# Kernel optimization log

Hardware: AMD Instinct MI355X
Metric: run time of the kernel (lower is better)

The kernel has to match this reference:

```python
import jax, jax.numpy as jnp
import numpy as np

D = 512        # input_dimension
STEPS = 6      # set2set processing steps
N = 100000     # set size (nodes)


def setup_inputs() -> dict:
    key = jax.random.key(0)
    ks = jax.random.split(key, 7)
    s_in = 1.0 / np.sqrt(2 * D)
    s_h = 1.0 / np.sqrt(D)
    s_p = 1.0 / np.sqrt(D * STEPS)
    return {
        "x": jax.random.normal(ks[0], (N, D), dtype=jnp.float32),
        # PyTorch LSTM params: W_ih [4D, 2D], W_hh [4D, D], gate order i,f,g,o
        "W_ih": jax.random.uniform(ks[1], (4 * D, 2 * D), jnp.float32, -s_in, s_in),
        "W_hh": jax.random.uniform(ks[2], (4 * D, D), jnp.float32, -s_h, s_h),
        "b_ih": jax.random.uniform(ks[3], (4 * D,), jnp.float32, -s_h, s_h),
        "b_hh": jax.random.uniform(ks[4], (4 * D,), jnp.float32, -s_h, s_h),
        # projection Linear(D*STEPS -> D)
        "W_proj": jax.random.uniform(ks[5], (D, D * STEPS), jnp.float32, -s_p, s_p),
        "b_proj": jax.random.uniform(ks[6], (D,), jnp.float32, -s_p, s_p),
    }


def reference(x, W_ih, W_hh, b_ih, b_hh, W_proj, b_proj):
    d = x.shape[1]
    h0 = jnp.zeros((d,), dtype=x.dtype)
    c0 = jnp.zeros((d,), dtype=x.dtype)

    def step(carry, _):
        h, c = carry
        scores = jax.nn.softmax(x @ h)          # [N] attention over the set
        ctx = scores @ x                         # [D] attended context
        inp = jnp.concatenate([ctx, h])          # [2D] lstm input (context, hidden)
        gates = W_ih @ inp + b_ih + W_hh @ h + b_hh  # [4D]
        i, f, g, o = jnp.split(gates, 4)
        i = jax.nn.sigmoid(i)
        f = jax.nn.sigmoid(f)
        g = jnp.tanh(g)
        o = jax.nn.sigmoid(o)
        c_new = f * c + i * g
        h_new = o * jnp.tanh(c_new)
        return (h_new, c_new), ctx

    (_, _), contexts = jax.lax.scan(step, (h0, c0), None, length=STEPS)  # [STEPS, D]
    return jax.nn.softmax(W_proj @ contexts.reshape(-1) + b_proj)  # [D]
```

## Files before the change

### kernel.cpp

```cpp
#include <hip/hip_runtime.h>
#include <math.h>

#define D 512
#define STEPS 6
#define MAXB1 1024

__device__ __forceinline__ float wave_reduce_sum(float v) {
#pragma unroll
    for (int off = 32; off > 0; off >>= 1) v += __shfl_xor(v, off);
    return v;
}

__device__ __forceinline__ float dot8(const float4& a, const float4& b,
                                      const float4& ha, const float4& hb) {
    return a.x*ha.x + a.y*ha.y + a.z*ha.z + a.w*ha.w
         + b.x*hb.x + b.y*hb.y + b.z*hb.z + b.w*hb.w;
}

#define ONLINE(dv, av, bv) do {                                          \
    if ((dv) > m) {                                                      \
        float sc_ = __expf(m - (dv));                                    \
        s *= sc_;                                                        \
        va.x *= sc_; va.y *= sc_; va.z *= sc_; va.w *= sc_;              \
        vb.x *= sc_; vb.y *= sc_; vb.z *= sc_; vb.w *= sc_;              \
        m = (dv);                                                        \
    }                                                                    \
    float w_ = __expf((dv) - m);                                         \
    s += w_;                                                             \
    va.x += w_*(av).x; va.y += w_*(av).y; va.z += w_*(av).z; va.w += w_*(av).w; \
    vb.x += w_*(bv).x; vb.y += w_*(bv).y; vb.z += w_*(bv).z; vb.w += w_*(bv).w; \
} while (0)

__global__ __launch_bounds__(256, 4) void attn_kernel(
    const float* __restrict__ x, const float* __restrict__ h,
    float* __restrict__ pm, float* __restrict__ ps, float* __restrict__ pv, int N)
{
    __shared__ float h_s[D];
    __shared__ float red_v[4][D];
    __shared__ float red_ms[8];
    for (int i = threadIdx.x; i < D; i += 256) h_s[i] = h[i];
    __syncthreads();

    const int wave = threadIdx.x >> 6, lane = threadIdx.x & 63;
    const int nw = gridDim.x << 2;
    const float4 ha = ((const float4*)h_s)[lane];
    const float4 hb = ((const float4*)h_s)[64 + lane];

    float m = -1e30f, s = 0.f;
    float4 va = make_float4(0.f, 0.f, 0.f, 0.f);
    float4 vb = make_float4(0.f, 0.f, 0.f, 0.f);

    int i = (blockIdx.x << 2) + wave;
    const int limit4 = N - 3 * nw;
    for (; i < limit4; i += (nw << 2)) {
        const float4* x0 = (const float4*)(x + (size_t)i * D);
        const float4* x1 = (const float4*)(x + (size_t)(i + nw) * D);
        const float4* x2 = (const float4*)(x + (size_t)(i + 2 * nw) * D);
        const float4* x3 = (const float4*)(x + (size_t)(i + 3 * nw) * D);
        float4 a0 = x0[lane], b0 = x0[64 + lane];
        float4 a1 = x1[lane], b1 = x1[64 + lane];
        float4 a2 = x2[lane], b2 = x2[64 + lane];
        float4 a3 = x3[lane], b3 = x3[64 + lane];
        float d0 = dot8(a0, b0, ha, hb);
        float d1 = dot8(a1, b1, ha, hb);
        float d2 = dot8(a2, b2, ha, hb);
        float d3 = dot8(a3, b3, ha, hb);
#pragma unroll
        for (int off = 32; off > 0; off >>= 1) {
            d0 += __shfl_xor(d0, off);
            d1 += __shfl_xor(d1, off);
            d2 += __shfl_xor(d2, off);
            d3 += __shfl_xor(d3, off);
        }
        ONLINE(d0, a0, b0);
        ONLINE(d1, a1, b1);
        ONLINE(d2, a2, b2);
        ONLINE(d3, a3, b3);
    }
    for (; i < N; i += nw) {
        const float4* x0 = (const float4*)(x + (size_t)i * D);
        float4 a0 = x0[lane], b0 = x0[64 + lane];
        float d0 = dot8(a0, b0, ha, hb);
        d0 = wave_reduce_sum(d0);
        ONLINE(d0, a0, b0);
    }

    ((float4*)red_v[wave])[lane] = va;
    ((float4*)red_v[wave])[64 + lane] = vb;
    if (lane == 0) { red_ms[wave] = m; red_ms[4 + wave] = s; }
    __syncthreads();

    float m0 = red_ms[0], m1 = red_ms[1], m2 = red_ms[2], m3 = red_ms[3];
    float bm = fmaxf(fmaxf(m0, m1), fmaxf(m2, m3));
    float sc0 = __expf(m0 - bm), sc1 = __expf(m1 - bm);
    float sc2 = __expf(m2 - bm), sc3 = __expf(m3 - bm);
    if (threadIdx.x == 0) {
        pm[blockIdx.x] = bm;
        ps[blockIdx.x] = red_ms[4]*sc0 + red_ms[5]*sc1 + red_ms[6]*sc2 + red_ms[7]*sc3;
    }
    const int t = threadIdx.x;
    float v0 = red_v[0][t]*sc0 + red_v[1][t]*sc1 + red_v[2][t]*sc2 + red_v[3][t]*sc3;
    float v1 = red_v[0][t+256]*sc0 + red_v[1][t+256]*sc1
             + red_v[2][t+256]*sc2 + red_v[3][t+256]*sc3;
    pv[(size_t)blockIdx.x * D + t] = v0;
    pv[(size_t)blockIdx.x * D + t + 256] = v1;
}

__global__ __launch_bounds__(256) void combine_kernel(
    const float* __restrict__ pm, const float* __restrict__ ps,
    const float* __restrict__ pv, float* __restrict__ ctx,
    float* __restrict__ ctx_store, int B1)
{
    __shared__ float sm[MAXB1];
    __shared__ float red[8];
    __shared__ float pr[4][64];
    const int tid = threadIdx.x, lane = tid & 63, wave = tid >> 6;

    float lm = -1e30f;
    for (int b = tid; b < B1; b += 256) lm = fmaxf(lm, pm[b]);
#pragma unroll
    for (int off = 32; off > 0; off >>= 1) lm = fmaxf(lm, __shfl_xor(lm, off));
    if (lane == 0) red[wave] = lm;
    __syncthreads();
    float M = fmaxf(fmaxf(red[0], red[1]), fmaxf(red[2], red[3]));

    float lS = 0.f;
    for (int b = tid; b < B1; b += 256) {
        float e = __expf(pm[b] - M);
        sm[b] = e;
        lS += ps[b] * e;
    }
#pragma unroll
    for (int off = 32; off > 0; off >>= 1) lS += __shfl_xor(lS, off);
    if (lane == 0) red[4 + wave] = lS;
    __syncthreads();
    float S = red[4] + red[5] + red[6] + red[7];

    const int d = (blockIdx.x << 6) + lane;
    float acc = 0.f;
    for (int b = wave; b < B1; b += 4)
        acc += pv[(size_t)b * D + d] * sm[b];
    pr[wave][lane] = acc;
    __syncthreads();
    if (tid < 64) {
        float v = (pr[0][lane] + pr[1][lane] + pr[2][lane] + pr[3][lane]) / S;
        int dd = (blockIdx.x << 6) + lane;
        ctx[dd] = v;
        ctx_store[dd] = v;
    }
}

__global__ __launch_bounds__(256) void lstm_kernel(
    const float* __restrict__ W_ih, const float* __restrict__ W_hh,
    const float* __restrict__ b_ih, const float* __restrict__ b_hh,
    const float* __restrict__ ctx, const float* __restrict__ h_in,
    float* __restrict__ h_out, float* __restrict__ c)
{
    __shared__ float inp[2 * D];
    __shared__ float gate[4];
    const int tid = threadIdx.x, lane = tid & 63, g = tid >> 6;
    const int j = blockIdx.x;
    for (int i = tid; i < D; i += 256) { inp[i] = ctx[i]; inp[D + i] = h_in[i]; }
    __syncthreads();

    const int row = (g << 9) + j;
    const float4* wr = (const float4*)(W_ih + (size_t)row * (2 * D));
    float dot = 0.f;
#pragma unroll
    for (int q = 0; q < 4; ++q) {
        float4 w4 = wr[lane + (q << 6)];
        float4 i4 = ((const float4*)inp)[lane + (q << 6)];
        dot += w4.x*i4.x + w4.y*i4.y + w4.z*i4.z + w4.w*i4.w;
    }
    const float4* wr2 = (const float4*)(W_hh + (size_t)row * D);
#pragma unroll
    for (int q = 0; q < 2; ++q) {
        float4 w4 = wr2[lane + (q << 6)];
        float4 i4 = ((const float4*)(inp + D))[lane + (q << 6)];
        dot += w4.x*i4.x + w4.y*i4.y + w4.z*i4.z + w4.w*i4.w;
    }
    dot = wave_reduce_sum(dot);
    if (lane == 0) gate[g] = dot + b_ih[row] + b_hh[row];
    __syncthreads();
    if (tid == 0) {
        float ig = 1.f / (1.f + __expf(-gate[0]));
        float fg = 1.f / (1.f + __expf(-gate[1]));
        float gg = tanhf(gate[2]);
        float og = 1.f / (1.f + __expf(-gate[3]));
        float cn = fg * c[j] + ig * gg;
        c[j] = cn;
        h_out[j] = og * tanhf(cn);
    }
}

__global__ __launch_bounds__(256) void proj_kernel(
    const float* __restrict__ W_proj, const float* __restrict__ b_proj,
    const float* __restrict__ ctxs, float* __restrict__ logits)
{
    __shared__ float cc[STEPS * D];
    const int tid = threadIdx.x, lane = tid & 63, g = tid >> 6;
    for (int i = tid; i < STEPS * D; i += 256) cc[i] = ctxs[i];
    __syncthreads();

    const int row = (blockIdx.x << 2) + g;
    const float4* wr = (const float4*)(W_proj + (size_t)row * (STEPS * D));
    float dot = 0.f;
#pragma unroll
    for (int q = 0; q < 12; ++q) {
        float4 w4 = wr[lane + (q << 6)];
        float4 i4 = ((const float4*)cc)[lane + (q << 6)];
        dot += w4.x*i4.x + w4.y*i4.y + w4.z*i4.z + w4.w*i4.w;
    }
    dot = wave_reduce_sum(dot);
    if (lane == 0) logits[row] = dot + b_proj[row];
}

__global__ void softmax512_kernel(const float* __restrict__ logits, float* __restrict__ out)
{
    __shared__ float red[8];
    const int tid = threadIdx.x, lane = tid & 63, wave = tid >> 6;
    float v = logits[tid];
    float m = v;
#pragma unroll
    for (int off = 32; off > 0; off >>= 1) m = fmaxf(m, __shfl_xor(m, off));
    if (lane == 0) red[wave] = m;
    __syncthreads();
    m = red[0];
#pragma unroll
    for (int k = 1; k < 8; ++k) m = fmaxf(m, red[k]);
    __syncthreads();
    float e = __expf(v - m);
    float s = e;
#pragma unroll
    for (int off = 32; off > 0; off >>= 1) s += __shfl_xor(s, off);
    if (lane == 0) red[wave] = s;
    __syncthreads();
    s = 0.f;
#pragma unroll
    for (int k = 0; k < 8; ++k) s += red[k];
    out[tid] = e / s;
}

extern "C" void kernel_launch(void* const* d_in, const int* in_sizes, int n_in,
                              void* d_out, int out_size, void* d_ws, size_t ws_size,
                              hipStream_t stream)
{
    const float* x      = (const float*)d_in[0];
    const float* W_ih   = (const float*)d_in[1];
    const float* W_hh   = (const float*)d_in[2];
    const float* b_ih   = (const float*)d_in[3];
    const float* b_hh   = (const float*)d_in[4];
    const float* W_proj = (const float*)d_in[5];
    const float* b_proj = (const float*)d_in[6];
    const int N = in_sizes[0] / D;

    float* ws     = (float*)d_ws;
    float* hbuf   = ws;
    float* c      = ws + 1024;
    float* ctx    = ws + 1536;
    float* ctxs   = ws + 2048;
    float* logits = ws + 5120;
    const size_t base = 5632;
    int B1 = MAXB1;
    if ((base + (size_t)B1 * (D + 2)) * sizeof(float) > ws_size) {
        B1 = (int)((ws_size / sizeof(float) - base) / (D + 2));
        if (B1 > MAXB1) B1 = MAXB1;
        if (B1 < 8) B1 = 8;
    }
    float* pm = ws + base;
    float* ps = pm + B1;
    float* pv = ps + B1;

    hipMemsetAsync(d_ws, 0, 1536 * sizeof(float), stream);

    for (int t = 0; t < STEPS; ++t) {
        float* h_in  = hbuf + ((t & 1) << 9);
        float* h_out = hbuf + (((t + 1) & 1) << 9);
        attn_kernel<<<B1, 256, 0, stream>>>(x, h_in, pm, ps, pv, N);
        combine_kernel<<<8, 256, 0, stream>>>(pm, ps, pv, ctx, ctxs + t * D, B1);
        lstm_kernel<<<512, 256, 0, stream>>>(W_ih, W_hh, b_ih, b_hh, ctx, h_in, h_out, c);
    }
    proj_kernel<<<128, 256, 0, stream>>>(W_proj, b_proj, ctxs, logits);
    softmax512_kernel<<<1, 512, 0, stream>>>(logits, (float*)d_out);
}
```

Before: 902.0 us.

## Fuse all set2set stages into one persistent cooperative kernel with grid syncs

Replaces the 20 separate launches (attention, combine and LSTM per step, then projection and softmax) with a single cooperative persistent kernel that uses grid.sync between stages. The goal is to remove per-launch overhead and gaps between launches. In exchange, the attention phase runs with fewer blocks (CUs times occupancy, at most 512), which may reduce memory-level parallelism on the 200MB x stream. The LSTM phase serialises gate rows per block with __syncthreads, and grid barriers cost time. The old multi-kernel path is kept as a fallback if the cooperative launch fails.

```diff
diff --git a/kernel.cpp b/kernel.cpp
--- a/kernel.cpp
+++ b/kernel.cpp
@@ -1,9 +1,21 @@
 #include <hip/hip_runtime.h>
+#include <hip/hip_cooperative_groups.h>
 #include <math.h>
+
+namespace cg = cooperative_groups;
 
 #define D 512
 #define STEPS 6
 #define MAXB1 1024
+
+#define WS_HBUF   0
+#define WS_C      1024
+#define WS_CTX    1536
+#define WS_CTXS   2048
+#define WS_LOGITS 5120
+#define WS_PM     5632
+#define WS_PS     6656
+#define WS_PV     7680
 
 __device__ __forceinline__ float wave_reduce_sum(float v) {
 #pragma unroll
@@ -30,6 +42,7 @@
     va.x += w_*(av).x; va.y += w_*(av).y; va.z += w_*(av).z; va.w += w_*(av).w; \
     vb.x += w_*(bv).x; vb.y += w_*(bv).y; vb.z += w_*(bv).z; vb.w += w_*(bv).w; \
 } while (0)
+
 
 __global__ __launch_bounds__(256, 4) void attn_kernel(
     const float* __restrict__ x, const float* __restrict__ h,
@@ -241,6 +254,238 @@
     out[tid] = e / s;
 }
 
+
+struct SharedU {
+    union {
+        struct { float h_s[D]; float red_v[4][D]; float red_ms[8]; } attn;
+        struct { float sm[512]; float red[8]; float pr[4][64]; } comb;
+        struct { float inp[2 * D]; float gate[4]; } lstm;
+        struct { float cc[STEPS * D]; } proj;
+    };
+};
+
+__global__ __launch_bounds__(256, 2) void s2s_kernel(
+    const float* __restrict__ x,
+    const float* __restrict__ W_ih, const float* __restrict__ W_hh,
+    const float* __restrict__ b_ih, const float* __restrict__ b_hh,
+    const float* __restrict__ W_proj, const float* __restrict__ b_proj,
+    float* __restrict__ out, float* __restrict__ ws, int N)
+{
+    cg::grid_group grid = cg::this_grid();
+    __shared__ SharedU su;
+
+    float* hbuf   = ws + WS_HBUF;
+    float* c      = ws + WS_C;
+    float* ctx    = ws + WS_CTX;
+    float* ctxs   = ws + WS_CTXS;
+    float* logits = ws + WS_LOGITS;
+    float* pm     = ws + WS_PM;
+    float* ps     = ws + WS_PS;
+    float* pv     = ws + WS_PV;
+
+    const int tid = threadIdx.x, lane = tid & 63, wave = tid >> 6;
+    const int bid = blockIdx.x;
+    const int NB = gridDim.x;
+    const int nw = NB << 2;
+
+    if (bid == 0)
+        for (int i = tid; i < 1536; i += 256) ws[i] = 0.f;
+    grid.sync();
+
+    for (int t = 0; t < STEPS; ++t) {
+        float* h_in  = hbuf + ((t & 1) << 9);
+        float* h_out = hbuf + (((t + 1) & 1) << 9);
+
+        {
+            for (int i = tid; i < D; i += 256) su.attn.h_s[i] = h_in[i];
+            __syncthreads();
+            const float4 ha = ((const float4*)su.attn.h_s)[lane];
+            const float4 hb = ((const float4*)su.attn.h_s)[64 + lane];
+
+            float m = -1e30f, s = 0.f;
+            float4 va = make_float4(0.f, 0.f, 0.f, 0.f);
+            float4 vb = make_float4(0.f, 0.f, 0.f, 0.f);
+
+            int i = (bid << 2) + wave;
+            const int limit4 = N - 3 * nw;
+            for (; i < limit4; i += (nw << 2)) {
+                const float4* x0 = (const float4*)(x + (size_t)i * D);
+                const float4* x1 = (const float4*)(x + (size_t)(i + nw) * D);
+                const float4* x2 = (const float4*)(x + (size_t)(i + 2 * nw) * D);
+                const float4* x3 = (const float4*)(x + (size_t)(i + 3 * nw) * D);
+                float4 a0 = x0[lane], b0 = x0[64 + lane];
+                float4 a1 = x1[lane], b1 = x1[64 + lane];
+                float4 a2 = x2[lane], b2 = x2[64 + lane];
+                float4 a3 = x3[lane], b3 = x3[64 + lane];
+                float d0 = dot8(a0, b0, ha, hb);
+                float d1 = dot8(a1, b1, ha, hb);
+                float d2 = dot8(a2, b2, ha, hb);
+                float d3 = dot8(a3, b3, ha, hb);
+#pragma unroll
+                for (int off = 32; off > 0; off >>= 1) {
+                    d0 += __shfl_xor(d0, off);
+                    d1 += __shfl_xor(d1, off);
+                    d2 += __shfl_xor(d2, off);
+                    d3 += __shfl_xor(d3, off);
+                }
+                ONLINE(d0, a0, b0);
+                ONLINE(d1, a1, b1);
+                ONLINE(d2, a2, b2);
+                ONLINE(d3, a3, b3);
+            }
+            for (; i < N; i += nw) {
+                const float4* x0 = (const float4*)(x + (size_t)i * D);
+                float4 a0 = x0[lane], b0 = x0[64 + lane];
+                float d0 = dot8(a0, b0, ha, hb);
+                d0 = wave_reduce_sum(d0);
+                ONLINE(d0, a0, b0);
+            }
+
+            ((float4*)su.attn.red_v[wave])[lane] = va;
+            ((float4*)su.attn.red_v[wave])[64 + lane] = vb;
+            if (lane == 0) { su.attn.red_ms[wave] = m; su.attn.red_ms[4 + wave] = s; }
+            __syncthreads();
+
+            float m0 = su.attn.red_ms[0], m1 = su.attn.red_ms[1];
+            float m2 = su.attn.red_ms[2], m3 = su.attn.red_ms[3];
+            float bm = fmaxf(fmaxf(m0, m1), fmaxf(m2, m3));
+            float sc0 = __expf(m0 - bm), sc1 = __expf(m1 - bm);
+            float sc2 = __expf(m2 - bm), sc3 = __expf(m3 - bm);
+            if (tid == 0) {
+                pm[bid] = bm;
+                ps[bid] = su.attn.red_ms[4]*sc0 + su.attn.red_ms[5]*sc1
+                        + su.attn.red_ms[6]*sc2 + su.attn.red_ms[7]*sc3;
+            }
+            float v0 = su.attn.red_v[0][tid]*sc0 + su.attn.red_v[1][tid]*sc1
+                     + su.attn.red_v[2][tid]*sc2 + su.attn.red_v[3][tid]*sc3;
+            float v1 = su.attn.red_v[0][tid+256]*sc0 + su.attn.red_v[1][tid+256]*sc1
+                     + su.attn.red_v[2][tid+256]*sc2 + su.attn.red_v[3][tid+256]*sc3;
+            pv[(size_t)bid * D + tid] = v0;
+            pv[(size_t)bid * D + tid + 256] = v1;
+        }
+        grid.sync();
+
+        if (bid < 8) {
+            float lm = -1e30f;
+            for (int b = tid; b < NB; b += 256) lm = fmaxf(lm, pm[b]);
+#pragma unroll
+            for (int off = 32; off > 0; off >>= 1) lm = fmaxf(lm, __shfl_xor(lm, off));
+            if (lane == 0) su.comb.red[wave] = lm;
+            __syncthreads();
+            float M = fmaxf(fmaxf(su.comb.red[0], su.comb.red[1]),
+                            fmaxf(su.comb.red[2], su.comb.red[3]));
+
+            float lS = 0.f;
+            for (int b = tid; b < NB; b += 256) {
+                float e = __expf(pm[b] - M);
+                su.comb.sm[b] = e;
+                lS += ps[b] * e;
+            }
+#pragma unroll
+            for (int off = 32; off > 0; off >>= 1) lS += __shfl_xor(lS, off);
+            if (lane == 0) su.comb.red[4 + wave] = lS;
+            __syncthreads();
+            float S = su.comb.red[4] + su.comb.red[5] + su.comb.red[6] + su.comb.red[7];
+
+            const int d = (bid << 6) + lane;
+            float acc = 0.f;
+            for (int b = wave; b < NB; b += 4)
+                acc += pv[(size_t)b * D + d] * su.comb.sm[b];
+            su.comb.pr[wave][lane] = acc;
+            __syncthreads();
+            if (tid < 64) {
+                float v = (su.comb.pr[0][lane] + su.comb.pr[1][lane]
+                         + su.comb.pr[2][lane] + su.comb.pr[3][lane]) / S;
+                ctx[d] = v;
+                ctxs[t * D + d] = v;
+            }
+        }
+        grid.sync();
+
+        {
+            for (int i = tid; i < D; i += 256) {
+                su.lstm.inp[i] = ctx[i];
+                su.lstm.inp[D + i] = h_in[i];
+            }
+            __syncthreads();
+
+            for (int j = bid; j < D; j += NB) {
+                const int row = (wave << 9) + j;
+                const float4* wr = (const float4*)(W_ih + (size_t)row * (2 * D));
+                float dot = 0.f;
+#pragma unroll
+                for (int q = 0; q < 4; ++q) {
+                    float4 w4 = wr[lane + (q << 6)];
+                    float4 i4 = ((const float4*)su.lstm.inp)[lane + (q << 6)];
+                    dot += w4.x*i4.x + w4.y*i4.y + w4.z*i4.z + w4.w*i4.w;
+                }
+                const float4* wr2 = (const float4*)(W_hh + (size_t)row * D);
+#pragma unroll
+                for (int q = 0; q < 2; ++q) {
+                    float4 w4 = wr2[lane + (q << 6)];
+                    float4 i4 = ((const float4*)(su.lstm.inp + D))[lane + (q << 6)];
+                    dot += w4.x*i4.x + w4.y*i4.y + w4.z*i4.z + w4.w*i4.w;
+                }
+                dot = wave_reduce_sum(dot);
+                if (lane == 0) su.lstm.gate[wave] = dot + b_ih[row] + b_hh[row];
+                __syncthreads();
+                if (tid == 0) {
+                    float ig = 1.f / (1.f + __expf(-su.lstm.gate[0]));
+                    float fg = 1.f / (1.f + __expf(-su.lstm.gate[1]));
+                    float gg = tanhf(su.lstm.gate[2]);
+                    float og = 1.f / (1.f + __expf(-su.lstm.gate[3]));
+                    float cn = fg * c[j] + ig * gg;
+                    c[j] = cn;
+                    h_out[j] = og * tanhf(cn);
+                }
+                __syncthreads();
+            }
+        }
+        grid.sync();
+    }
+
+    {
+        for (int i = tid; i < STEPS * D; i += 256) su.proj.cc[i] = ctxs[i];
+        __syncthreads();
+        for (int rg = bid; rg < 128; rg += NB) {
+            const int row = (rg << 2) + wave;
+            const float4* wr = (const float4*)(W_proj + (size_t)row * (STEPS * D));
+            float dot = 0.f;
+#pragma unroll
+            for (int q = 0; q < 12; ++q) {
+                float4 w4 = wr[lane + (q << 6)];
+                float4 i4 = ((const float4*)su.proj.cc)[lane + (q << 6)];
+                dot += w4.x*i4.x + w4.y*i4.y + w4.z*i4.z + w4.w*i4.w;
+            }
+            dot = wave_reduce_sum(dot);
+            if (lane == 0) logits[row] = dot + b_proj[row];
+        }
+    }
+    grid.sync();
+
+    if (bid == 0) {
+        float v0 = logits[tid], v1 = logits[tid + 256];
+        float m = fmaxf(v0, v1);
+#pragma unroll
+        for (int off = 32; off > 0; off >>= 1) m = fmaxf(m, __shfl_xor(m, off));
+        if (lane == 0) su.comb.red[wave] = m;
+        __syncthreads();
+        m = fmaxf(fmaxf(su.comb.red[0], su.comb.red[1]),
+                  fmaxf(su.comb.red[2], su.comb.red[3]));
+        __syncthreads();
+        float e0 = __expf(v0 - m), e1 = __expf(v1 - m);
+        float ls = e0 + e1;
+#pragma unroll
+        for (int off = 32; off > 0; off >>= 1) ls += __shfl_xor(ls, off);
+        if (lane == 0) su.comb.red[4 + wave] = ls;
+        __syncthreads();
+        float S = su.comb.red[4] + su.comb.red[5] + su.comb.red[6] + su.comb.red[7];
+        out[tid] = e0 / S;
+        out[tid + 256] = e1 / S;
+    }
+}
+
+
 extern "C" void kernel_launch(void* const* d_in, const int* in_sizes, int n_in,
                               void* d_out, int out_size, void* d_ws, size_t ws_size,
                               hipStream_t stream)
@@ -252,34 +497,48 @@
     const float* b_hh   = (const float*)d_in[4];
     const float* W_proj = (const float*)d_in[5];
     const float* b_proj = (const float*)d_in[6];
-    const int N = in_sizes[0] / D;
-
-    float* ws     = (float*)d_ws;
-    float* hbuf   = ws;
-    float* c      = ws + 1024;
-    float* ctx    = ws + 1536;
-    float* ctxs   = ws + 2048;
-    float* logits = ws + 5120;
-    const size_t base = 5632;
-    int B1 = MAXB1;
-    if ((base + (size_t)B1 * (D + 2)) * sizeof(float) > ws_size) {
-        B1 = (int)((ws_size / sizeof(float) - base) / (D + 2));
-        if (B1 > MAXB1) B1 = MAXB1;
-        if (B1 < 8) B1 = 8;
-    }
-    float* pm = ws + base;
-    float* ps = pm + B1;
-    float* pv = ps + B1;
-
-    hipMemsetAsync(d_ws, 0, 1536 * sizeof(float), stream);
-
-    for (int t = 0; t < STEPS; ++t) {
-        float* h_in  = hbuf + ((t & 1) << 9);
-        float* h_out = hbuf + (((t + 1) & 1) << 9);
-        attn_kernel<<<B1, 256, 0, stream>>>(x, h_in, pm, ps, pv, N);
-        combine_kernel<<<8, 256, 0, stream>>>(pm, ps, pv, ctx, ctxs + t * D, B1);
-        lstm_kernel<<<512, 256, 0, stream>>>(W_ih, W_hh, b_ih, b_hh, ctx, h_in, h_out, c);
-    }
-    proj_kernel<<<128, 256, 0, stream>>>(W_proj, b_proj, ctxs, logits);
-    softmax512_kernel<<<1, 512, 0, stream>>>(logits, (float*)d_out);
-}
+    float* out          = (float*)d_out;
+    float* ws           = (float*)d_ws;
+    int N = in_sizes[0] / D;
+
+    int dev = 0;
+    (void)hipGetDevice(&dev);
+    int cus = 256;
+    (void)hipDeviceGetAttribute(&cus, hipDeviceAttributeMultiprocessorCount, dev);
+    int maxb = 0;
+    if (hipOccupancyMaxActiveBlocksPerMultiprocessor(&maxb, (const void*)s2s_kernel,
+                                                     256, 0) != hipSuccess || maxb < 1)
+        maxb = 1;
+    long long Gll = (long long)cus * maxb;
+    int G = (Gll > 512) ? 512 : (int)Gll;
+    if (G < 8) G = 8;
+
+    void* args[] = { (void*)&x, (void*)&W_ih, (void*)&W_hh, (void*)&b_ih,
+                     (void*)&b_hh, (void*)&W_proj, (void*)&b_proj,
+                     (void*)&out, (void*)&ws, (void*)&N };
+    hipError_t e = hipLaunchCooperativeKernel((void*)s2s_kernel, dim3(G), dim3(256),
+                                              args, 0, stream);
+    if (e != hipSuccess) {
+        (void)hipGetLastError();
+        float* hbuf   = ws + WS_HBUF;
+        float* c      = ws + WS_C;
+        float* ctx    = ws + WS_CTX;
+        float* ctxs   = ws + WS_CTXS;
+        float* logits = ws + WS_LOGITS;
+        float* pm     = ws + WS_PM;
+        float* ps     = ws + WS_PS;
+        float* pv     = ws + WS_PV;
+        const int B1 = MAXB1;
+
+        hipMemsetAsync(d_ws, 0, 1536 * sizeof(float), stream);
+        for (int t = 0; t < STEPS; ++t) {
+            float* h_in  = hbuf + ((t & 1) << 9);
+            float* h_out = hbuf + (((t + 1) & 1) << 9);
+            attn_kernel<<<B1, 256, 0, stream>>>(x, h_in, pm, ps, pv, N);
+            combine_kernel<<<8, 256, 0, stream>>>(pm, ps, pv, ctx, ctxs + t * D, B1);
+            lstm_kernel<<<512, 256, 0, stream>>>(W_ih, W_hh, b_ih, b_hh, ctx, h_in, h_out, c);
+        }
+        proj_kernel<<<128, 256, 0, stream>>>(W_proj, b_proj, ctxs, logits);
+        softmax512_kernel<<<1, 512, 0, stream>>>(logits, (float*)d_out);
+    }
+}
```

Measured after the change: 1.708 ms. +89.4%, slower.

## Fuse all set2set stages into one persistent kernel with grid barriers

Applied to the files above, without the earlier changes.

Replaces the 20 separate launches (attention, combine, LSTM per step, then projection and softmax) with one persistent kernel. Its grid is sized from occupancy, and phases are separated by atomic-counter grid barriers. The online-softmax update is also made branch-free. This removes launch overhead and per-kernel tail drain between the many small dependent stages. The cost is a spin-wait barrier that depends on all blocks being co-resident. The LSTM work is also spread over fewer blocks, since at most G blocks loop over 512 rows.

```diff
diff --git a/kernel.cpp b/kernel.cpp
--- a/kernel.cpp
+++ b/kernel.cpp
@@ -3,7 +3,17 @@
 
 #define D 512
 #define STEPS 6
-#define MAXB1 1024
+#define MAXG 1024
+
+#define WS_BAR    0
+#define WS_HBUF   32
+#define WS_C      1056
+#define WS_CTX    1568
+#define WS_CTXS   2080
+#define WS_LOGITS 5152
+#define WS_PM     5664
+#define WS_PS     6688
+#define WS_PV     7712
 
 __device__ __forceinline__ float wave_reduce_sum(float v) {
 #pragma unroll
@@ -17,228 +27,259 @@
          + b.x*hb.x + b.y*hb.y + b.z*hb.z + b.w*hb.w;
 }
 
-#define ONLINE(dv, av, bv) do {                                          \
-    if ((dv) > m) {                                                      \
-        float sc_ = __expf(m - (dv));                                    \
-        s *= sc_;                                                        \
-        va.x *= sc_; va.y *= sc_; va.z *= sc_; va.w *= sc_;              \
-        vb.x *= sc_; vb.y *= sc_; vb.z *= sc_; vb.w *= sc_;              \
-        m = (dv);                                                        \
-    }                                                                    \
-    float w_ = __expf((dv) - m);                                         \
-    s += w_;                                                             \
-    va.x += w_*(av).x; va.y += w_*(av).y; va.z += w_*(av).z; va.w += w_*(av).w; \
-    vb.x += w_*(bv).x; vb.y += w_*(bv).y; vb.z += w_*(bv).z; vb.w += w_*(bv).w; \
+#define ONLINE_BF(dv, av, bv) do {                                       \
+    float nm_ = fmaxf(m, (dv));                                          \
+    float sc_ = __expf(m - nm_);          \
+    float w_  = __expf((dv) - nm_);                                      \
+    m = nm_;                                                             \
+    s = s * sc_ + w_;                                                    \
+    va.x = va.x*sc_ + w_*(av).x; va.y = va.y*sc_ + w_*(av).y;            \
+    va.z = va.z*sc_ + w_*(av).z; va.w = va.w*sc_ + w_*(av).w;            \
+    vb.x = vb.x*sc_ + w_*(bv).x; vb.y = vb.y*sc_ + w_*(bv).y;            \
+    vb.z = vb.z*sc_ + w_*(bv).z; vb.w = vb.w*sc_ + w_*(bv).w;            \
 } while (0)
 
-__global__ __launch_bounds__(256, 4) void attn_kernel(
-    const float* __restrict__ x, const float* __restrict__ h,
-    float* __restrict__ pm, float* __restrict__ ps, float* __restrict__ pv, int N)
-{
-    __shared__ float h_s[D];
-    __shared__ float red_v[4][D];
-    __shared__ float red_ms[8];
-    for (int i = threadIdx.x; i < D; i += 256) h_s[i] = h[i];
+__device__ __forceinline__ void gbar(unsigned* cnt, unsigned NB) {
     __syncthreads();
-
-    const int wave = threadIdx.x >> 6, lane = threadIdx.x & 63;
-    const int nw = gridDim.x << 2;
-    const float4 ha = ((const float4*)h_s)[lane];
-    const float4 hb = ((const float4*)h_s)[64 + lane];
-
-    float m = -1e30f, s = 0.f;
-    float4 va = make_float4(0.f, 0.f, 0.f, 0.f);
-    float4 vb = make_float4(0.f, 0.f, 0.f, 0.f);
-
-    int i = (blockIdx.x << 2) + wave;
-    const int limit4 = N - 3 * nw;
-    for (; i < limit4; i += (nw << 2)) {
-        const float4* x0 = (const float4*)(x + (size_t)i * D);
-        const float4* x1 = (const float4*)(x + (size_t)(i + nw) * D);
-        const float4* x2 = (const float4*)(x + (size_t)(i + 2 * nw) * D);
-        const float4* x3 = (const float4*)(x + (size_t)(i + 3 * nw) * D);
-        float4 a0 = x0[lane], b0 = x0[64 + lane];
-        float4 a1 = x1[lane], b1 = x1[64 + lane];
-        float4 a2 = x2[lane], b2 = x2[64 + lane];
-        float4 a3 = x3[lane], b3 = x3[64 + lane];
-        float d0 = dot8(a0, b0, ha, hb);
-        float d1 = dot8(a1, b1, ha, hb);
-        float d2 = dot8(a2, b2, ha, hb);
-        float d3 = dot8(a3, b3, ha, hb);
-#pragma unroll
-        for (int off = 32; off > 0; off >>= 1) {
-            d0 += __shfl_xor(d0, off);
-            d1 += __shfl_xor(d1, off);
-            d2 += __shfl_xor(d2, off);
-            d3 += __shfl_xor(d3, off);
-        }
-        ONLINE(d0, a0, b0);
-        ONLINE(d1, a1, b1);
-        ONLINE(d2, a2, b2);
-        ONLINE(d3, a3, b3);
+    if (threadIdx.x == 0) {
+        __threadfence();
+        atomicAdd(cnt, 1u);
+        int spins = 0;
+        while (__hip_atomic_load(cnt, __ATOMIC_RELAXED,
+                                 __HIP_MEMORY_SCOPE_AGENT) < NB) {
+            __builtin_amdgcn_s_sleep(2);
+            if (++spins > (1 << 22)) break;
+        }
+        __threadfence();
     }
-    for (; i < N; i += nw) {
-        const float4* x0 = (const float4*)(x + (size_t)i * D);
-        float4 a0 = x0[lane], b0 = x0[64 + lane];
-        float d0 = dot8(a0, b0, ha, hb);
-        d0 = wave_reduce_sum(d0);
-        ONLINE(d0, a0, b0);
-    }
-
-    ((float4*)red_v[wave])[lane] = va;
-    ((float4*)red_v[wave])[64 + lane] = vb;
-    if (lane == 0) { red_ms[wave] = m; red_ms[4 + wave] = s; }
     __syncthreads();
-
-    float m0 = red_ms[0], m1 = red_ms[1], m2 = red_ms[2], m3 = red_ms[3];
-    float bm = fmaxf(fmaxf(m0, m1), fmaxf(m2, m3));
-    float sc0 = __expf(m0 - bm), sc1 = __expf(m1 - bm);
-    float sc2 = __expf(m2 - bm), sc3 = __expf(m3 - bm);
-    if (threadIdx.x == 0) {
-        pm[blockIdx.x] = bm;
-        ps[blockIdx.x] = red_ms[4]*sc0 + red_ms[5]*sc1 + red_ms[6]*sc2 + red_ms[7]*sc3;
-    }
-    const int t = threadIdx.x;
-    float v0 = red_v[0][t]*sc0 + red_v[1][t]*sc1 + red_v[2][t]*sc2 + red_v[3][t]*sc3;
-    float v1 = red_v[0][t+256]*sc0 + red_v[1][t+256]*sc1
-             + red_v[2][t+256]*sc2 + red_v[3][t+256]*sc3;
-    pv[(size_t)blockIdx.x * D + t] = v0;
-    pv[(size_t)blockIdx.x * D + t + 256] = v1;
-}
-
-__global__ __launch_bounds__(256) void combine_kernel(
-    const float* __restrict__ pm, const float* __restrict__ ps,
-    const float* __restrict__ pv, float* __restrict__ ctx,
-    float* __restrict__ ctx_store, int B1)
-{
-    __shared__ float sm[MAXB1];
-    __shared__ float red[8];
-    __shared__ float pr[4][64];
-    const int tid = threadIdx.x, lane = tid & 63, wave = tid >> 6;
-
-    float lm = -1e30f;
-    for (int b = tid; b < B1; b += 256) lm = fmaxf(lm, pm[b]);
-#pragma unroll
-    for (int off = 32; off > 0; off >>= 1) lm = fmaxf(lm, __shfl_xor(lm, off));
-    if (lane == 0) red[wave] = lm;
-    __syncthreads();
-    float M = fmaxf(fmaxf(red[0], red[1]), fmaxf(red[2], red[3]));
-
-    float lS = 0.f;
-    for (int b = tid; b < B1; b += 256) {
-        float e = __expf(pm[b] - M);
-        sm[b] = e;
-        lS += ps[b] * e;
-    }
-#pragma unroll
-    for (int off = 32; off > 0; off >>= 1) lS += __shfl_xor(lS, off);
-    if (lane == 0) red[4 + wave] = lS;
-    __syncthreads();
-    float S = red[4] + red[5] + red[6] + red[7];
-
-    const int d = (blockIdx.x << 6) + lane;
-    float acc = 0.f;
-    for (int b = wave; b < B1; b += 4)
-        acc += pv[(size_t)b * D + d] * sm[b];
-    pr[wave][lane] = acc;
-    __syncthreads();
-    if (tid < 64) {
-        float v = (pr[0][lane] + pr[1][lane] + pr[2][lane] + pr[3][lane]) / S;
-        int dd = (blockIdx.x << 6) + lane;
-        ctx[dd] = v;
-        ctx_store[dd] = v;
-    }
-}
-
-__global__ __launch_bounds__(256) void lstm_kernel(
+}
+
+struct SharedU {
+    union {
+        struct { float h_s[D]; float red_v[4][D]; float red_ms[8]; } attn;
+        struct { float sm[MAXG]; float red[8]; float pr[4][64]; } comb;
+        struct { float inp[2 * D]; float gate[4]; } lstm;
+        struct { float cc[STEPS * D]; } proj;
+    };
+};
+
+__global__ __launch_bounds__(256, 4) void s2s_kernel(
+    const float* __restrict__ x,
     const float* __restrict__ W_ih, const float* __restrict__ W_hh,
     const float* __restrict__ b_ih, const float* __restrict__ b_hh,
-    const float* __restrict__ ctx, const float* __restrict__ h_in,
-    float* __restrict__ h_out, float* __restrict__ c)
+    const float* __restrict__ W_proj, const float* __restrict__ b_proj,
+    float* __restrict__ out, float* __restrict__ ws, int N)
 {
-    __shared__ float inp[2 * D];
-    __shared__ float gate[4];
-    const int tid = threadIdx.x, lane = tid & 63, g = tid >> 6;
-    const int j = blockIdx.x;
-    for (int i = tid; i < D; i += 256) { inp[i] = ctx[i]; inp[D + i] = h_in[i]; }
-    __syncthreads();
-
-    const int row = (g << 9) + j;
-    const float4* wr = (const float4*)(W_ih + (size_t)row * (2 * D));
-    float dot = 0.f;
-#pragma unroll
-    for (int q = 0; q < 4; ++q) {
-        float4 w4 = wr[lane + (q << 6)];
-        float4 i4 = ((const float4*)inp)[lane + (q << 6)];
-        dot += w4.x*i4.x + w4.y*i4.y + w4.z*i4.z + w4.w*i4.w;
+    __shared__ SharedU su;
+
+    unsigned* bar  = (unsigned*)(ws + WS_BAR);
+    float* hbuf    = ws + WS_HBUF;
+    float* c       = ws + WS_C;
+    float* ctx     = ws + WS_CTX;
+    float* ctxs    = ws + WS_CTXS;
+    float* logits  = ws + WS_LOGITS;
+    float* pm      = ws + WS_PM;
+    float* ps      = ws + WS_PS;
+    float* pv      = ws + WS_PV;
+
+    const int tid = threadIdx.x, lane = tid & 63, wave = tid >> 6;
+    const int bid = blockIdx.x;
+    const unsigned NB = gridDim.x;
+    const int nw = (int)NB << 2;
+    int bslot = 0;
+
+    for (int t = 0; t < STEPS; ++t) {
+        float* h_in  = hbuf + ((t & 1) << 9);
+        float* h_out = hbuf + (((t + 1) & 1) << 9);
+
+        {
+            for (int i = tid; i < D; i += 256) su.attn.h_s[i] = h_in[i];
+            __syncthreads();
+            const float4 ha = ((const float4*)su.attn.h_s)[lane];
+            const float4 hb = ((const float4*)su.attn.h_s)[64 + lane];
+
+            float m = -1e30f, s = 0.f;
+            float4 va = make_float4(0.f, 0.f, 0.f, 0.f);
+            float4 vb = make_float4(0.f, 0.f, 0.f, 0.f);
+
+            int i = (bid << 2) + wave;
+            const int limit4 = N - 3 * nw;
+            for (; i < limit4; i += (nw << 2)) {
+                const float4* x0 = (const float4*)(x + (size_t)i * D);
+                const float4* x1 = (const float4*)(x + (size_t)(i + nw) * D);
+                const float4* x2 = (const float4*)(x + (size_t)(i + 2 * nw) * D);
+                const float4* x3 = (const float4*)(x + (size_t)(i + 3 * nw) * D);
+                float4 a0 = x0[lane], b0 = x0[64 + lane];
+                float4 a1 = x1[lane], b1 = x1[64 + lane];
+                float4 a2 = x2[lane], b2 = x2[64 + lane];
+                float4 a3 = x3[lane], b3 = x3[64 + lane];
+                float d0 = dot8(a0, b0, ha, hb);
+                float d1 = dot8(a1, b1, ha, hb);
+                float d2 = dot8(a2, b2, ha, hb);
+                float d3 = dot8(a3, b3, ha, hb);
+#pragma unroll
+                for (int off = 32; off > 0; off >>= 1) {
+                    d0 += __shfl_xor(d0, off);
+                    d1 += __shfl_xor(d1, off);
+                    d2 += __shfl_xor(d2, off);
+                    d3 += __shfl_xor(d3, off);
+                }
+                ONLINE_BF(d0, a0, b0);
+                ONLINE_BF(d1, a1, b1);
+                ONLINE_BF(d2, a2, b2);
+                ONLINE_BF(d3, a3, b3);
+            }
+            for (; i < N; i += nw) {
+                const float4* x0 = (const float4*)(x + (size_t)i * D);
+                float4 a0 = x0[lane], b0 = x0[64 + lane];
+                float d0 = dot8(a0, b0, ha, hb);
+                d0 = wave_reduce_sum(d0);
+                ONLINE_BF(d0, a0, b0);
+            }
+
+            ((float4*)su.attn.red_v[wave])[lane] = va;
+            ((float4*)su.attn.red_v[wave])[64 + lane] = vb;
+            if (lane == 0) { su.attn.red_ms[wave] = m; su.attn.red_ms[4 + wave] = s; }
+            __syncthreads();
+
+            float m0 = su.attn.red_ms[0], m1 = su.attn.red_ms[1];
+            float m2 = su.attn.red_ms[2], m3 = su.attn.red_ms[3];
+            float bm = fmaxf(fmaxf(m0, m1), fmaxf(m2, m3));
+            float sc0 = __expf(m0 - bm), sc1 = __expf(m1 - bm);
+            float sc2 = __expf(m2 - bm), sc3 = __expf(m3 - bm);
+            if (tid == 0) {
+                pm[bid] = bm;
+                ps[bid] = su.attn.red_ms[4]*sc0 + su.attn.red_ms[5]*sc1
+                        + su.attn.red_ms[6]*sc2 + su.attn.red_ms[7]*sc3;
+            }
+            float v0 = su.attn.red_v[0][tid]*sc0 + su.attn.red_v[1][tid]*sc1
+                     + su.attn.red_v[2][tid]*sc2 + su.attn.red_v[3][tid]*sc3;
+            float v1 = su.attn.red_v[0][tid+256]*sc0 + su.attn.red_v[1][tid+256]*sc1
+                     + su.attn.red_v[2][tid+256]*sc2 + su.attn.red_v[3][tid+256]*sc3;
+            pv[(size_t)bid * D + tid] = v0;
+            pv[(size_t)bid * D + tid + 256] = v1;
+        }
+        gbar(&bar[bslot++], NB);
+
+        if (bid < 8) {
+            float lm = -1e30f;
+            for (int b = tid; b < (int)NB; b += 256) lm = fmaxf(lm, pm[b]);
+#pragma unroll
+            for (int off = 32; off > 0; off >>= 1) lm = fmaxf(lm, __shfl_xor(lm, off));
+            if (lane == 0) su.comb.red[wave] = lm;
+            __syncthreads();
+            float M = fmaxf(fmaxf(su.comb.red[0], su.comb.red[1]),
+                            fmaxf(su.comb.red[2], su.comb.red[3]));
+
+            float lS = 0.f;
+            for (int b = tid; b < (int)NB; b += 256) {
+                float e = __expf(pm[b] - M);
+                su.comb.sm[b] = e;
+                lS += ps[b] * e;
+            }
+#pragma unroll
+            for (int off = 32; off > 0; off >>= 1) lS += __shfl_xor(lS, off);
+            if (lane == 0) su.comb.red[4 + wave] = lS;
+            __syncthreads();
+            float S = su.comb.red[4] + su.comb.red[5] + su.comb.red[6] + su.comb.red[7];
+
+            const int d = (bid << 6) + lane;
+            float acc = 0.f;
+            for (int b = wave; b < (int)NB; b += 4)
+                acc += pv[(size_t)b * D + d] * su.comb.sm[b];
+            su.comb.pr[wave][lane] = acc;
+            __syncthreads();
+            if (tid < 64) {
+                float v = (su.comb.pr[0][lane] + su.comb.pr[1][lane]
+                         + su.comb.pr[2][lane] + su.comb.pr[3][lane]) / S;
+                ctx[d] = v;
+                ctxs[t * D + d] = v;
+            }
+        }
+        gbar(&bar[bslot++], NB);
+
+        {
+            for (int i = tid; i < D; i += 256) {
+                su.lstm.inp[i] = ctx[i];
+                su.lstm.inp[D + i] = h_in[i];
+            }
+            __syncthreads();
+
+            for (int j = bid; j < D; j += (int)NB) {
+                const int row = (wave << 9) + j;
+                const float4* wr = (const float4*)(W_ih + (size_t)row * (2 * D));
+                float dot = 0.f;
+#pragma unroll
+                for (int q = 0; q < 4; ++q) {
+                    float4 w4 = wr[lane + (q << 6)];
+                    float4 i4 = ((const float4*)su.lstm.inp)[lane + (q << 6)];
+                    dot += w4.x*i4.x + w4.y*i4.y + w4.z*i4.z + w4.w*i4.w;
+                }
+                const float4* wr2 = (const float4*)(W_hh + (size_t)row * D);
+#pragma unroll
+                for (int q = 0; q < 2; ++q) {
+                    float4 w4 = wr2[lane + (q << 6)];
+                    float4 i4 = ((const float4*)(su.lstm.inp + D))[lane + (q << 6)];
+                    dot += w4.x*i4.x + w4.y*i4.y + w4.z*i4.z + w4.w*i4.w;
+                }
+                dot = wave_reduce_sum(dot);
+                if (lane == 0) su.lstm.gate[wave] = dot + b_ih[row] + b_hh[row];
+                __syncthreads();
+                if (tid == 0) {
+                    float ig = 1.f / (1.f + __expf(-su.lstm.gate[0]));
+                    float fg = 1.f / (1.f + __expf(-su.lstm.gate[1]));
+                    float gg = tanhf(su.lstm.gate[2]);
+                    float og = 1.f / (1.f + __expf(-su.lstm.gate[3]));
+                    float cn = fg * c[j] + ig * gg;
+                    c[j] = cn;
+                    h_out[j] = og * tanhf(cn);
+                }
+                __syncthreads();
+            }
+        }
+        gbar(&bar[bslot++], NB);
     }
-    const float4* wr2 = (const float4*)(W_hh + (size_t)row * D);
-#pragma unroll
-    for (int q = 0; q < 2; ++q) {
-        float4 w4 = wr2[lane + (q << 6)];
-        float4 i4 = ((const float4*)(inp + D))[lane + (q << 6)];
-        dot += w4.x*i4.x + w4.y*i4.y + w4.z*i4.z + w4.w*i4.w;
+
+    {
+        for (int i = tid; i < STEPS * D; i += 256) su.proj.cc[i] = ctxs[i];
+        __syncthreads();
+        for (int rg = bid; rg < 128; rg += (int)NB) {
+            const int row = (rg << 2) + wave;
+            const float4* wr = (const float4*)(W_proj + (size_t)row * (STEPS * D));
+            float dot = 0.f;
+#pragma unroll
+            for (int q = 0; q < 12; ++q) {
+                float4 w4 = wr[lane + (q << 6)];
+                float4 i4 = ((const float4*)su.proj.cc)[lane + (q << 6)];
+                dot += w4.x*i4.x + w4.y*i4.y + w4.z*i4.z + w4.w*i4.w;
+            }
+            dot = wave_reduce_sum(dot);
+            if (lane == 0) logits[row] = dot + b_proj[row];
+        }
     }
-    dot = wave_reduce_sum(dot);
-    if (lane == 0) gate[g] = dot + b_ih[row] + b_hh[row];
-    __syncthreads();
-    if (tid == 0) {
-        float ig = 1.f / (1.f + __expf(-gate[0]));
-        float fg = 1.f / (1.f + __expf(-gate[1]));
-        float gg = tanhf(gate[2]);
-        float og = 1.f / (1.f + __expf(-gate[3]));
-        float cn = fg * c[j] + ig * gg;
-        c[j] = cn;
-        h_out[j] = og * tanhf(cn);
+    gbar(&bar[bslot++], NB);
+
+    if (bid == 0) {
+        float v0 = logits[tid], v1 = logits[tid + 256];
+        float m = fmaxf(v0, v1);
+#pragma unroll
+        for (int off = 32; off > 0; off >>= 1) m = fmaxf(m, __shfl_xor(m, off));
+        if (lane == 0) su.comb.red[wave] = m;
+        __syncthreads();
+        m = fmaxf(fmaxf(su.comb.red[0], su.comb.red[1]),
+                  fmaxf(su.comb.red[2], su.comb.red[3]));
+        __syncthreads();
+        float e0 = __expf(v0 - m), e1 = __expf(v1 - m);
+        float ls = e0 + e1;
+#pragma unroll
+        for (int off = 32; off > 0; off >>= 1) ls += __shfl_xor(ls, off);
+        if (lane == 0) su.comb.red[4 + wave] = ls;
+        __syncthreads();
+        float S = su.comb.red[4] + su.comb.red[5] + su.comb.red[6] + su.comb.red[7];
+        out[tid] = e0 / S;
+        out[tid + 256] = e1 / S;
     }
-}
-
-__global__ __launch_bounds__(256) void proj_kernel(
-    const float* __restrict__ W_proj, const float* __restrict__ b_proj,
-    const float* __restrict__ ctxs, float* __restrict__ logits)
-{
-    __shared__ float cc[STEPS * D];
-    const int tid = threadIdx.x, lane = tid & 63, g = tid >> 6;
-    for (int i = tid; i < STEPS * D; i += 256) cc[i] = ctxs[i];
-    __syncthreads();
-
-    const int row = (blockIdx.x << 2) + g;
-    const float4* wr = (const float4*)(W_proj + (size_t)row * (STEPS * D));
-    float dot = 0.f;
-#pragma unroll
-    for (int q = 0; q < 12; ++q) {
-        float4 w4 = wr[lane + (q << 6)];
-        float4 i4 = ((const float4*)cc)[lane + (q << 6)];
-        dot += w4.x*i4.x + w4.y*i4.y + w4.z*i4.z + w4.w*i4.w;
-    }
-    dot = wave_reduce_sum(dot);
-    if (lane == 0) logits[row] = dot + b_proj[row];
-}
-
-__global__ void softmax512_kernel(const float* __restrict__ logits, float* __restrict__ out)
-{
-    __shared__ float red[8];
-    const int tid = threadIdx.x, lane = tid & 63, wave = tid >> 6;
-    float v = logits[tid];
-    float m = v;
-#pragma unroll
-    for (int off = 32; off > 0; off >>= 1) m = fmaxf(m, __shfl_xor(m, off));
-    if (lane == 0) red[wave] = m;
-    __syncthreads();
-    m = red[0];
-#pragma unroll
-    for (int k = 1; k < 8; ++k) m = fmaxf(m, red[k]);
-    __syncthreads();
-    float e = __expf(v - m);
-    float s = e;
-#pragma unroll
-    for (int off = 32; off > 0; off >>= 1) s += __shfl_xor(s, off);
-    if (lane == 0) red[wave] = s;
-    __syncthreads();
-    s = 0.f;
-#pragma unroll
-    for (int k = 0; k < 8; ++k) s += red[k];
-    out[tid] = e / s;
 }
 
 extern "C" void kernel_launch(void* const* d_in, const int* in_sizes, int n_in,
@@ -252,34 +293,24 @@
     const float* b_hh   = (const float*)d_in[4];
     const float* W_proj = (const float*)d_in[5];
     const float* b_proj = (const float*)d_in[6];
-    const int N = in_sizes[0] / D;
-
-    float* ws     = (float*)d_ws;
-    float* hbuf   = ws;
-    float* c      = ws + 1024;
-    float* ctx    = ws + 1536;
-    float* ctxs   = ws + 2048;
-    float* logits = ws + 5120;
-    const size_t base = 5632;
-    int B1 = MAXB1;
-    if ((base + (size_t)B1 * (D + 2)) * sizeof(float) > ws_size) {
-        B1 = (int)((ws_size / sizeof(float) - base) / (D + 2));
-        if (B1 > MAXB1) B1 = MAXB1;
-        if (B1 < 8) B1 = 8;
-    }
-    float* pm = ws + base;
-    float* ps = pm + B1;
-    float* pv = ps + B1;
-
-    hipMemsetAsync(d_ws, 0, 1536 * sizeof(float), stream);
-
-    for (int t = 0; t < STEPS; ++t) {
-        float* h_in  = hbuf + ((t & 1) << 9);
-        float* h_out = hbuf + (((t + 1) & 1) << 9);
-        attn_kernel<<<B1, 256, 0, stream>>>(x, h_in, pm, ps, pv, N);
-        combine_kernel<<<8, 256, 0, stream>>>(pm, ps, pv, ctx, ctxs + t * D, B1);
-        lstm_kernel<<<512, 256, 0, stream>>>(W_ih, W_hh, b_ih, b_hh, ctx, h_in, h_out, c);
-    }
-    proj_kernel<<<128, 256, 0, stream>>>(W_proj, b_proj, ctxs, logits);
-    softmax512_kernel<<<1, 512, 0, stream>>>(logits, (float*)d_out);
-}
+    float* out          = (float*)d_out;
+    float* ws           = (float*)d_ws;
+    int N = in_sizes[0] / D;
+
+    int dev = 0;
+    (void)hipGetDevice(&dev);
+    int cus = 256;
+    (void)hipDeviceGetAttribute(&cus, hipDeviceAttributeMultiprocessorCount, dev);
+    int maxb = 0;
+    if (hipOccupancyMaxActiveBlocksPerMultiprocessor(&maxb, (const void*)s2s_kernel,
+                                                     256, 0) != hipSuccess || maxb < 1)
+        maxb = 1;
+    long long Gll = (long long)cus * maxb;
+    int G = (Gll > MAXG) ? MAXG : (int)Gll;
+    if (G < 8) G = 8;
+
+    hipMemsetAsync(d_ws, 0, (32 + 1024 + 512) * sizeof(float), stream);
+
+    s2s_kernel<<<dim3(G), dim3(256), 0, stream>>>(x, W_ih, W_hh, b_ih, b_hh,
+                                                  W_proj, b_proj, out, ws, N);
+}
```

New measurement: 1.450 ms. 1.61x slower.
